# Kernel optimization log

Hardware: AMD Instinct MI355X
Metric: run time of the kernel (lower is better)

## Reference

```python
import jax, jax.numpy as jnp
import numpy as np

D_MODEL = 1024
D_FF = 4096
FFN_H = int(2 * D_FF / 3)  # 2730, per SwiGLUMLP
B, S = 4, 4096
LN_EPS = 1e-5
ATTN_EPS = 1e-6


def layer_norm(x, g, b):
    mu = jnp.mean(x, axis=-1, keepdims=True)
    var = jnp.mean(jnp.square(x - mu), axis=-1, keepdims=True)
    return (x - mu) * jax.lax.rsqrt(var + LN_EPS) * g + b


def setup_inputs() -> dict:
    key = jax.random.key(0)
    ks = jax.random.split(key, 16)
    s = 0.02
    return {
        "x": jax.random.normal(ks[0], (B, S, D_MODEL), dtype=jnp.float32),
        "Wqkv": jax.random.normal(ks[1], (D_MODEL, 3 * D_MODEL), dtype=jnp.float32) * s,
        "bqkv": jnp.zeros((3 * D_MODEL,), jnp.float32),
        "Wg": jax.random.normal(ks[2], (D_MODEL, FFN_H), dtype=jnp.float32) * s,
        "bg": jnp.zeros((FFN_H,), jnp.float32),
        "Wu": jax.random.normal(ks[3], (D_MODEL, FFN_H), dtype=jnp.float32) * s,
        "bu": jnp.zeros((FFN_H,), jnp.float32),
        "Wd": jax.random.normal(ks[4], (FFN_H, D_MODEL), dtype=jnp.float32) * s,
        "bd": jnp.zeros((D_MODEL,), jnp.float32),
        "g1": jnp.ones((D_MODEL,), jnp.float32),
        "b1": jnp.zeros((D_MODEL,), jnp.float32),
        "g2": jnp.ones((D_MODEL,), jnp.float32),
        "b2": jnp.zeros((D_MODEL,), jnp.float32),
    }


def reference(x, Wqkv, bqkv, Wg, bg, Wu, bu, Wd, bd, g1, b1, g2, b2):
    # QKV projection, split into q, k, v (each [B,S,D])
    qkv = jnp.einsum("bsd,de->bse", x, Wqkv) + bqkv
    q, k, v = jnp.split(qkv, 3, axis=-1)

    # Linear attention with elu(x)+1 feature map (non-causal)
    qp = jax.nn.elu(q) + 1.0
    kp = jax.nn.elu(k) + 1.0
    kv = jnp.einsum("bsd,bse->bde", kp, v)        # [B,D,D] context
    num = jnp.einsum("bsd,bde->bse", qp, kv)       # [B,S,D]
    k_sum = jnp.sum(kp, axis=1)                    # [B,D]
    den = jnp.einsum("bsd,bd->bs", qp, k_sum)[..., None]
    attn = num / (den + ATTN_EPS)

    x = layer_norm(x + attn, g1, b1)

    # SwiGLU MLP
    gate = jnp.einsum("bsd,dh->bsh", x, Wg) + bg
    up = jnp.einsum("bsd,dh->bsh", x, Wu) + bu
    ffn = jnp.einsum("bsh,hd->bsd", jax.nn.silu(gate) * up, Wd) + bd

    return layer_norm(x + ffn, g2, b2)
```

## Files before the change

kernel.cpp:

```cpp
#include <hip/hip_runtime.h>

#define SEQ 4096
#define TOK 16384
#define DM 1024
#define NQKV 3072
#define FFH 2730
#define FFHP 2816

typedef __bf16 bf16x8 __attribute__((ext_vector_type(8)));
typedef float f32x4 __attribute__((ext_vector_type(4)));

__device__ __forceinline__ unsigned short f2bf(float f) {
  union { float f; unsigned u; } v; v.f = f;
  unsigned r = v.u + 0x7fffu + ((v.u >> 16) & 1u);
  return (unsigned short)(r >> 16);
}
__device__ __forceinline__ float bf2f(unsigned short h) {
  union { unsigned u; float f; } v; v.u = ((unsigned)h) << 16;
  return v.f;
}

__device__ __forceinline__ void xcd_swizzle(int& bx, int& by) {
  const int gx = gridDim.x, gy = gridDim.y;
  const int chunk = gy >> 3;
  const int csh = __ffs(chunk) - 1;
  const int lin = by * gx + bx;
  const int xcd = lin & 7, j = lin >> 3;
  by = xcd * chunk + (j & (chunk - 1));
  bx = j >> csh;
}

enum { M_QKV = 0, M_BF16 = 1, M_NUM = 2, M_BIAS_F32 = 5 };

template<int MODE>
__global__ __launch_bounds__(256)
void gemm_kernel(const unsigned short* __restrict__ A,
                 const unsigned short* __restrict__ BT,
                 int K, int lda, int ldb, int ldc,
                 long zsA, long zsB, long zsC,
                 void* __restrict__ out0, void* __restrict__ out1, void* __restrict__ out2,
                 const float* __restrict__ bias, int nbias)
{
  __shared__ unsigned short As[2][128 * 64];
  __shared__ unsigned short Bs[2][128 * 64];
  const int tid  = threadIdx.x;
  const int wave = tid >> 6, lane = tid & 63;
  const int quad = lane >> 4, l16 = lane & 15;
  const int bz = blockIdx.z;
  int bx = blockIdx.x, by = blockIdx.y;
  xcd_swizzle(bx, by);

  const unsigned short* Ab = A + (size_t)zsA * bz + (size_t)by * 128 * lda;
  const unsigned short* Bb = BT + (size_t)zsB * bz + (size_t)bx * 128 * ldb;

  f32x4 acc[4][4] = {};

  const int srow   = lane >> 3;
  const int scol_g = (((lane & 7) ^ srow) * 8);
  const int axor   = l16 & 7;

  auto stage = [&](int buf, int k0) {
#pragma unroll
    for (int j = 0; j < 4; ++j) {
      int c = wave * 4 + j;
      const unsigned short* sa = Ab + (size_t)(c * 8 + srow) * lda + k0 + scol_g;
      __builtin_amdgcn_global_load_lds((__attribute__((address_space(1))) void*)sa,
          (__attribute__((address_space(3))) void*)(As[buf] + c * 512), 16, 0, 0);
      const unsigned short* sb = Bb + (size_t)(c * 8 + srow) * ldb + k0 + scol_g;
      __builtin_amdgcn_global_load_lds((__attribute__((address_space(1))) void*)sb,
          (__attribute__((address_space(3))) void*)(Bs[buf] + c * 512), 16, 0, 0);
    }
  };

  const int NIT = K >> 6;
  stage(0, 0);
  int cur = 0;
  for (int it = 0; it < NIT; ++it) {
    __builtin_amdgcn_s_waitcnt(0);
    __syncthreads();
    if (it + 1 < NIT) stage(cur ^ 1, (it + 1) << 6);
#pragma unroll
    for (int kk = 0; kk < 64; kk += 32) {
      bf16x8 af[4], bfr[4];
#pragma unroll
      for (int mt = 0; mt < 4; ++mt)
        af[mt] = *(const bf16x8*)(As[cur] + ((wave >> 1) * 64 + mt * 16 + l16) * 64
                                     + ((((kk >> 3) + quad) ^ axor) * 8));
#pragma unroll
      for (int nt = 0; nt < 4; ++nt)
        bfr[nt] = *(const bf16x8*)(Bs[cur] + ((wave & 1) * 64 + nt * 16 + l16) * 64
                                      + ((((kk >> 3) + quad) ^ axor) * 8));
#pragma unroll
      for (int mt = 0; mt < 4; ++mt)
#pragma unroll
        for (int nt = 0; nt < 4; ++nt)
          acc[mt][nt] = __builtin_amdgcn_mfma_f32_16x16x32_bf16(af[mt], bfr[nt], acc[mt][nt], 0, 0, 0);
    }
    cur ^= 1;
  }

#pragma unroll
  for (int mt = 0; mt < 4; ++mt) {
#pragma unroll
    for (int nt = 0; nt < 4; ++nt) {
      const int r0 = by * 128 + (wave >> 1) * 64 + mt * 16 + quad * 4;
      const int c  = bx * 128 + (wave & 1) * 64 + nt * 16 + l16;
      float vals[4];
#pragma unroll
      for (int i = 0; i < 4; ++i) vals[i] = acc[mt][nt][i];

      if (MODE == M_QKV) {
        const int b = r0 >> 12, s0 = r0 & 4095;
#pragma unroll
        for (int i = 0; i < 4; ++i) vals[i] += bias[c];
        if (c < 1024) {
#pragma unroll
          for (int i = 0; i < 4; ++i) {
            float e = vals[i] > 0.f ? vals[i] + 1.f : __expf(vals[i]);
            ((unsigned short*)out0)[(size_t)(r0 + i) * DM + c] = f2bf(e);
          }
        } else if (c < 2048) {
          ushort4 o;
          float e0 = vals[0] > 0.f ? vals[0] + 1.f : __expf(vals[0]);
          float e1 = vals[1] > 0.f ? vals[1] + 1.f : __expf(vals[1]);
          float e2 = vals[2] > 0.f ? vals[2] + 1.f : __expf(vals[2]);
          float e3 = vals[3] > 0.f ? vals[3] + 1.f : __expf(vals[3]);
          o.x = f2bf(e0); o.y = f2bf(e1); o.z = f2bf(e2); o.w = f2bf(e3);
          *(ushort4*)((unsigned short*)out1 + (size_t)b * DM * SEQ + (size_t)(c - 1024) * SEQ + s0) = o;
        } else {
          ushort4 o;
          o.x = f2bf(vals[0]); o.y = f2bf(vals[1]); o.z = f2bf(vals[2]); o.w = f2bf(vals[3]);
          *(ushort4*)((unsigned short*)out2 + (size_t)b * DM * SEQ + (size_t)(c - 2048) * SEQ + s0) = o;
        }
      } else {
#pragma unroll
        for (int i = 0; i < 4; ++i) {
          const int r = r0 + i;
          float val = vals[i];
          if (MODE == M_BF16 || MODE == M_NUM) {
            ((unsigned short*)out0)[(size_t)zsC * bz + (size_t)r * ldc + c] = f2bf(val);
          } else {
            if (c < nbias) val += bias[c];
            ((float*)out0)[(size_t)r * ldc + c] = val;
          }
        }
      }
    }
  }
}

enum { G_GATEUP = 0, G_NUM = 1, G_BIAS_F32 = 2, G_QKV = 3 };

#define MBAR() asm volatile("s_barrier" ::: "memory")
#define WAITV(N) asm volatile("s_waitcnt vmcnt(" #N ")" ::: "memory")

#define LDS_ALL(BUF) do {                                                     \
    _Pragma("unroll")                                                         \
    for (int mt = 0; mt < 4; ++mt) {                                          \
      _Pragma("unroll")                                                       \
      for (int k2 = 0; k2 < 2; ++k2)                                          \
        af[0][mt][k2] = *(const bf16x8*)(As[BUF] +                            \
            (wm * 128 + mt * 16 + l16) * 64 + (((k2 * 4 + quad) ^ axor) * 8));\
    }                                                                         \
    _Pragma("unroll")                                                         \
    for (int nt = 0; nt < 2; ++nt) {                                          \
      _Pragma("unroll")                                                       \
      for (int k2 = 0; k2 < 2; ++k2)                                          \
        bfr[0][nt][k2] = *(const bf16x8*)(Bs[BUF] +                           \
            (wn * 64 + nt * 16 + l16) * 64 + (((k2 * 4 + quad) ^ axor) * 8)); \
    }                                                                         \
    _Pragma("unroll")                                                         \
    for (int mt = 0; mt < 4; ++mt) {                                          \
      _Pragma("unroll")                                                       \
      for (int k2 = 0; k2 < 2; ++k2)                                          \
        af[1][mt][k2] = *(const bf16x8*)(As[BUF] +                            \
            (wm * 128 + (4 + mt) * 16 + l16) * 64 +                           \
            (((k2 * 4 + quad) ^ axor) * 8));                                  \
    }                                                                         \
    _Pragma("unroll")                                                         \
    for (int nt = 0; nt < 2; ++nt) {                                          \
      _Pragma("unroll")                                                       \
      for (int k2 = 0; k2 < 2; ++k2)                                          \
        bfr[1][nt][k2] = *(const bf16x8*)(Bs[BUF] +                           \
            (wn * 64 + (2 + nt) * 16 + l16) * 64 +                            \
            (((k2 * 4 + quad) ^ axor) * 8));                                  \
    }                                                                         \
  } while (0)

#define MMAQ(QM, QN) do {                                                     \
    _Pragma("unroll")                                                         \
    for (int mt = 0; mt < 4; ++mt) {                                          \
      _Pragma("unroll")                                                       \
      for (int nt = 0; nt < 2; ++nt) {                                        \
        _Pragma("unroll")                                                     \
        for (int k2 = 0; k2 < 2; ++k2)                                        \
          acc[(QM) * 4 + mt][(QN) * 2 + nt] =                                 \
              __builtin_amdgcn_mfma_f32_16x16x32_bf16(af[QM][mt][k2],         \
                  bfr[QN][nt][k2], acc[(QM) * 4 + mt][(QN) * 2 + nt], 0, 0, 0);\
      }                                                                       \
    }                                                                         \
  } while (0)

#define PHASE(QM, QN, STAGE) do {                                             \
    STAGE                                                                     \
    MBAR();                                                                   \
    __builtin_amdgcn_sched_barrier(0);                                        \
    __builtin_amdgcn_s_setprio(1);                                            \
    MMAQ(QM, QN);                                                             \
    __builtin_amdgcn_s_setprio(0);                                            \
    WAITV(6);                                                                 \
    MBAR();                                                                   \
  } while (0)

template<int MODE>
__global__ __launch_bounds__(512, 2)
void gemm256_kernel(const unsigned short* __restrict__ A,
                    const unsigned short* __restrict__ BT,
                    int K, int lda, int ldb, int ldc,
                    long zsA, long zsB, long zsC,
                    void* __restrict__ out0,
                    void* __restrict__ out1, void* __restrict__ out2,
                    const float* __restrict__ bias0,
                    const float* __restrict__ bias1,
                    int nbias)
{
  __shared__ unsigned short As[2][256 * 64];
  __shared__ unsigned short Bs[2][256 * 64];
  const int tid  = threadIdx.x;
  const int wave = tid >> 6, lane = tid & 63;
  const int quad = lane >> 4, l16 = lane & 15;
  const int wm = wave >> 2, wn = wave & 3;
  const int bz = blockIdx.z;
  int bx = blockIdx.x, by = blockIdx.y;
  xcd_swizzle(bx, by);

  const unsigned short* Ab = A + (size_t)zsA * bz + (size_t)by * 256 * lda;
  const unsigned short* Bb = BT + (size_t)zsB * bz + (size_t)bx * 256 * ldb;

  f32x4 acc[8][4] = {};

  const int srow = lane >> 3;
  const int sxor = ((lane & 7) ^ srow) * 8;
  const int axor = l16 & 7;

  const unsigned short* pA[2][2];
  const unsigned short* pB[2][2];
  int cA[2][2], cB[2][2];
#pragma unroll
  for (int part = 0; part < 2; ++part) {
#pragma unroll
    for (int j = 0; j < 2; ++j) {
      int idx = wave * 2 + j;
      int ca = ((idx & 8) ? idx + 8 : idx) + part * 8;
      int cb = (idx >> 2) * 8 + (idx & 3) + part * 4;
      cA[part][j] = ca; cB[part][j] = cb;
      pA[part][j] = Ab + (size_t)(ca * 8 + srow) * lda + sxor;
      pB[part][j] = Bb + (size_t)(cb * 8 + srow) * ldb + sxor;
    }
  }

  auto stageA = [&](int buf, int part, int tile) {
    const int k0 = tile << 6;
#pragma unroll
    for (int j = 0; j < 2; ++j)
      __builtin_amdgcn_global_load_lds(
          (__attribute__((address_space(1))) void*)(pA[part][j] + k0),
          (__attribute__((address_space(3))) void*)(As[buf] + cA[part][j] * 512), 16, 0, 0);
  };
  auto stageB = [&](int buf, int part, int tile) {
    const int k0 = tile << 6;
#pragma unroll
    for (int j = 0; j < 2; ++j)
      __builtin_amdgcn_global_load_lds(
          (__attribute__((address_space(1))) void*)(pB[part][j] + k0),
          (__attribute__((address_space(3))) void*)(Bs[buf] + cB[part][j] * 512), 16, 0, 0);
  };

  stageA(0, 0, 0); stageB(0, 0, 0); stageA(0, 1, 0); stageB(0, 1, 0);
  stageA(1, 0, 1); stageB(1, 0, 1); stageA(1, 1, 1);
  WAITV(6);
  MBAR();

  bf16x8 af[2][4][2], bfr[2][2][2];
  const int NT = K >> 6;
  for (int i = 0; i < NT; i += 2) {
    const int t2s = (i + 2 < NT), t3s = (i + 3 < NT);
    LDS_ALL(0);
    PHASE(0, 0, { stageB(1, 1, i + 1); });
    PHASE(1, 0, { if (t2s) stageA(0, 0, i + 2); });
    PHASE(1, 1, { if (t2s) stageB(0, 0, i + 2); });
    PHASE(0, 1, { if (t2s) stageA(0, 1, i + 2); });
    LDS_ALL(1);
    PHASE(0, 0, { if (t2s) stageB(0, 1, i + 2); });
    PHASE(1, 0, { if (t3s) stageA(1, 0, i + 3); });
    PHASE(1, 1, { if (t3s) stageB(1, 0, i + 3); });
    PHASE(0, 1, { if (t3s) stageA(1, 1, i + 3); });
  }

  if (MODE == G_GATEUP) {
#pragma unroll
    for (int mt = 0; mt < 8; ++mt) {
      const int r0 = by * 256 + wm * 128 + mt * 16 + quad * 4;
#pragma unroll
      for (int p = 0; p < 2; ++p) {
        const int hc = bx * 128 + wn * 32 + p * 16 + l16;
        const float bgv = (hc < nbias) ? bias0[hc] : 0.f;
        const float buv = (hc < nbias) ? bias1[hc] : 0.f;
#pragma unroll
        for (int i2 = 0; i2 < 4; ++i2) {
          float g = acc[mt][2 * p][i2] + bgv;
          float u = acc[mt][2 * p + 1][i2] + buv;
          float hv = g / (1.f + __expf(-g)) * u;
          ((unsigned short*)out0)[(size_t)(r0 + i2) * ldc + hc] = f2bf(hv);
        }
      }
    }
  } else {
#pragma unroll
    for (int mt = 0; mt < 8; ++mt) {
#pragma unroll
      for (int nt = 0; nt < 4; ++nt) {
        const int r0 = by * 256 + wm * 128 + mt * 16 + quad * 4;
        const int c  = bx * 256 + wn * 64 + nt * 16 + l16;
#pragma unroll
        for (int i2 = 0; i2 < 4; ++i2) {
          float v = acc[mt][nt][i2];
          if (MODE == G_NUM) {
            ((unsigned short*)out0)[(size_t)zsC * bz + (size_t)(r0 + i2) * ldc + c] = f2bf(v);
          } else {
            if (c < nbias) v += bias0[c];
            ((float*)out0)[(size_t)(r0 + i2) * ldc + c] = v;
          }
        }
      }
    }
  }
}

__global__ __launch_bounds__(256)
void cvt_kernel(const float* __restrict__ in, unsigned short* __restrict__ out, int n)
{
  int i = (blockIdx.x * 256 + threadIdx.x) * 4;
  if (i < n) {
    float4 v = *(const float4*)(in + i);
    ushort4 o;
    o.x = f2bf(v.x); o.y = f2bf(v.y); o.z = f2bf(v.z); o.w = f2bf(v.w);
    *(ushort4*)(out + i) = o;
  }
}

__global__ __launch_bounds__(256)
void wtrans_kernel(const float* __restrict__ in, unsigned short* __restrict__ out,
                   int R, int C, int Cpad, int Rpad, int omode)
{
  __shared__ float tile[32][33];
  int r0 = blockIdx.x * 32;
  int c0 = blockIdx.y * 32;
  int tid = threadIdx.x;
#pragma unroll
  for (int j = 0; j < 4; ++j) {
    int r = j * 8 + (tid >> 5), c = tid & 31;
    float v = 0.f;
    if (r0 + r < R && c0 + c < C) v = in[(size_t)(r0 + r) * C + c0 + c];
    tile[r][c] = v;
  }
  __syncthreads();
#pragma unroll
  for (int j = 0; j < 4; ++j) {
    int c = j * 8 + (tid >> 5), r = tid & 31;
    int oc = c0 + c;
    int orow = (omode == 0) ? oc
             : ((oc >> 4) * 32 + (oc & 15) + ((omode == 2) ? 16 : 0));
    out[(size_t)orow * Rpad + (r0 + r)] = f2bf(tile[r][c]);
  }
}

__device__ __forceinline__ float block_sum(float v, float* sm)
{
#pragma unroll
  for (int o = 32; o > 0; o >>= 1) v += __shfl_down(v, o, 64);
  int w = threadIdx.x >> 6;
  if ((threadIdx.x & 63) == 0) sm[w] = v;
  __syncthreads();
  float r = sm[0] + sm[1] + sm[2] + sm[3];
  __syncthreads();
  return r;
}

__global__ __launch_bounds__(256)
void ksum_kernel(const unsigned short* __restrict__ kpT, float* __restrict__ ksum)
{
  __shared__ float sm[4];
  int row = blockIdx.x;
  const ushort4* src = (const ushort4*)(kpT + (size_t)row * SEQ);
  float s = 0.f;
#pragma unroll
  for (int j = 0; j < 4; ++j) {
    ushort4 v = src[threadIdx.x + j * 256];
    s += bf2f(v.x) + bf2f(v.y) + bf2f(v.z) + bf2f(v.w);
  }
  float tot = block_sum(s, sm);
  if (threadIdx.x == 0) ksum[row] = tot;
}

__global__ __launch_bounds__(256)
void ln1_kernel(const unsigned short* __restrict__ xb16, const unsigned short* __restrict__ num16,
                const unsigned short* __restrict__ qp, const float* __restrict__ ksum,
                const float* __restrict__ g1, const float* __restrict__ b1,
                unsigned short* __restrict__ yb)
{
  __shared__ float sm[4];
  int t = blockIdx.x, tid = threadIdx.x, b = t >> 12;
  ushort4 xv = ((const ushort4*)(xb16 + (size_t)t * DM))[tid];
  ushort4 nv = ((const ushort4*)(num16 + (size_t)t * DM))[tid];
  ushort4 qv = ((const ushort4*)(qp + (size_t)t * DM))[tid];
  float4 kv = ((const float4*)(ksum + (size_t)b * DM))[tid];
  float q0 = bf2f(qv.x), q1 = bf2f(qv.y), q2 = bf2f(qv.z), q3 = bf2f(qv.w);
  float den = block_sum(q0 * kv.x + q1 * kv.y + q2 * kv.z + q3 * kv.w, sm);
  float inv = 1.f / (den + 1e-6f);
  float r0 = bf2f(xv.x) + bf2f(nv.x) * inv, r1 = bf2f(xv.y) + bf2f(nv.y) * inv;
  float r2 = bf2f(xv.z) + bf2f(nv.z) * inv, r3 = bf2f(xv.w) + bf2f(nv.w) * inv;
  float s1 = block_sum(r0 + r1 + r2 + r3, sm);
  float s2 = block_sum(r0 * r0 + r1 * r1 + r2 * r2 + r3 * r3, sm);
  float mu = s1 * (1.f / 1024.f);
  float var = s2 * (1.f / 1024.f) - mu * mu;
  float rs = rsqrtf(var + 1e-5f);
  float4 gv = ((const float4*)g1)[tid];
  float4 bv = ((const float4*)b1)[tid];
  ushort4 o;
  o.x = f2bf((r0 - mu) * rs * gv.x + bv.x);
  o.y = f2bf((r1 - mu) * rs * gv.y + bv.y);
  o.z = f2bf((r2 - mu) * rs * gv.z + bv.z);
  o.w = f2bf((r3 - mu) * rs * gv.w + bv.w);
  ((ushort4*)(yb + (size_t)t * DM))[tid] = o;
}

__global__ __launch_bounds__(256)
void ln2_kernel(const unsigned short* __restrict__ yb, const float* __restrict__ ffn,
                const float* __restrict__ g2, const float* __restrict__ b2,
                float* __restrict__ out)
{
  __shared__ float sm[4];
  int t = blockIdx.x, tid = threadIdx.x;
  ushort4 yv = ((const ushort4*)(yb + (size_t)t * DM))[tid];
  float4 fv = ((const float4*)(ffn + (size_t)t * DM))[tid];
  float r0 = bf2f(yv.x) + fv.x, r1 = bf2f(yv.y) + fv.y;
  float r2 = bf2f(yv.z) + fv.z, r3 = bf2f(yv.w) + fv.w;
  float s1 = block_sum(r0 + r1 + r2 + r3, sm);
  float s2 = block_sum(r0 * r0 + r1 * r1 + r2 * r2 + r3 * r3, sm);
  float mu = s1 * (1.f / 1024.f);
  float var = s2 * (1.f / 1024.f) - mu * mu;
  float rs = rsqrtf(var + 1e-5f);
  float4 gv = ((const float4*)g2)[tid];
  float4 bv = ((const float4*)b2)[tid];
  float4 o;
  o.x = (r0 - mu) * rs * gv.x + bv.x;
  o.y = (r1 - mu) * rs * gv.y + bv.y;
  o.z = (r2 - mu) * rs * gv.z + bv.z;
  o.w = (r3 - mu) * rs * gv.w + bv.w;
  ((float4*)(out + (size_t)t * DM))[tid] = o;
}

extern "C" void kernel_launch(void* const* d_in, const int* in_sizes, int n_in,
                              void* d_out, int out_size, void* d_ws, size_t ws_size,
                              hipStream_t stream)
{
  const float* x    = (const float*)d_in[0];
  const float* Wqkv = (const float*)d_in[1];
  const float* bqkv = (const float*)d_in[2];
  const float* Wg   = (const float*)d_in[3];
  const float* bg   = (const float*)d_in[4];
  const float* Wu   = (const float*)d_in[5];
  const float* bu   = (const float*)d_in[6];
  const float* Wd   = (const float*)d_in[7];
  const float* bd   = (const float*)d_in[8];
  const float* g1   = (const float*)d_in[9];
  const float* b1   = (const float*)d_in[10];
  const float* g2   = (const float*)d_in[11];
  const float* b2   = (const float*)d_in[12];
  float* out = (float*)d_out;

  char* ws = (char*)d_ws;
  size_t off = 0;
  auto alloc = [&](size_t bytes) {
    char* p = ws + off;
    off += (bytes + 255) & ~(size_t)255;
    return p;
  };
  unsigned short* WqkvT = (unsigned short*)alloc((size_t)NQKV * DM * 2);
  unsigned short* WguT  = (unsigned short*)alloc((size_t)2 * FFHP * DM * 2);
  unsigned short* WdT   = (unsigned short*)alloc((size_t)DM * FFHP * 2);
  float*          ksum  = (float*)alloc((size_t)4 * DM * 4);
  unsigned short* xbyb  = (unsigned short*)alloc((size_t)TOK * DM * 2);
  unsigned short* kvT   = (unsigned short*)alloc((size_t)4 * DM * DM * 2);
  char* R3 = alloc((size_t)3 * TOK * DM * 2);
  unsigned short* qp  = (unsigned short*)(R3);
  unsigned short* kpT = (unsigned short*)(R3 + (size_t)TOK * DM * 2);
  unsigned short* vT  = (unsigned short*)(R3 + (size_t)2 * TOK * DM * 2);
  unsigned short* hbuf = (unsigned short*)(R3);
  unsigned short* xb = xbyb;
  unsigned short* yb = xbyb;
  unsigned short* num = (unsigned short*)d_out;
  float* ffn = (float*)d_out;

  dim3 blk(256), blk5(512);

  cvt_kernel<<<dim3(TOK * DM / 1024), blk, 0, stream>>>(x, xb, TOK * DM);
  wtrans_kernel<<<dim3(32, 96), blk, 0, stream>>>(Wqkv, WqkvT, 1024, 3072, 3072, 1024, 0);
  wtrans_kernel<<<dim3(32, 88), blk, 0, stream>>>(Wg, WguT, 1024, FFH, FFHP, 1024, 1);
  wtrans_kernel<<<dim3(32, 88), blk, 0, stream>>>(Wu, WguT, 1024, FFH, FFHP, 1024, 2);
  wtrans_kernel<<<dim3(88, 32), blk, 0, stream>>>(Wd, WdT, FFH, 1024, 1024, FFHP, 0);
  gemm_kernel<M_QKV><<<dim3(NQKV / 128, TOK / 128), blk, 0, stream>>>(
      xb, WqkvT, 1024, 1024, 1024, 0, 0, 0, 0, qp, kpT, vT, bqkv, NQKV);
  ksum_kernel<<<dim3(4096), blk, 0, stream>>>(kpT, ksum);
  gemm_kernel<M_BF16><<<dim3(8, 8, 4), blk, 0, stream>>>(
      vT, kpT, 4096, 4096, 4096, 1024,
      (long)DM * SEQ, (long)DM * SEQ, (long)DM * DM,
      kvT, nullptr, nullptr, nullptr, 0);
  gemm256_kernel<G_NUM><<<dim3(4, 16, 4), blk5, 0, stream>>>(
      qp, kvT, 1024, 1024, 1024, 1024,
      (long)SEQ * DM, (long)DM * DM, (long)SEQ * DM,
      num, nullptr, nullptr, nullptr, nullptr, 0);
  ln1_kernel<<<dim3(TOK), blk, 0, stream>>>(xb, num, qp, ksum, g1, b1, yb);
  gemm256_kernel<G_GATEUP><<<dim3(2 * FFHP / 256, TOK / 256), blk5, 0, stream>>>(
      yb, WguT, 1024, DM, DM, FFHP, 0, 0, 0, hbuf, nullptr, nullptr, bg, bu, FFH);
  gemm256_kernel<G_BIAS_F32><<<dim3(DM / 256, TOK / 256), blk5, 0, stream>>>(
      hbuf, WdT, FFHP, FFHP, FFHP, DM, 0, 0, 0, ffn, nullptr, nullptr, bd, nullptr, DM);
  ln2_kernel<<<dim3(TOK), blk, 0, stream>>>(yb, ffn, g2, b2, out);

  (void)in_sizes; (void)n_in; (void)out_size; (void)ws_size;
}
```

Baseline: 821.0 us.

## Stage gate-up epilogue through LDS for coalesced stores; defer vmcnt waits

The SwiGLU epilogue of the gate/up GEMM now writes bf16 results into a swizzled LDS tile, then each thread stores 16-byte vectors of contiguous columns to global memory. This replaces scattered 2-byte stores. The pipeline also drops the vmcnt wait from every phase, keeping it only before the LDS reload at the end of each half-iteration, and drains fully on the last tiles. This aims to cut stall time inside the main loop, with a small risk of reading stale LDS if the staging order is wrong. Unused out1/out2 parameters and an enum value are removed.

```diff
diff --git a/kernel.cpp b/kernel.cpp
--- a/kernel.cpp
+++ b/kernel.cpp
@@ -9,6 +9,7 @@
 
 typedef __bf16 bf16x8 __attribute__((ext_vector_type(8)));
 typedef float f32x4 __attribute__((ext_vector_type(4)));
+typedef unsigned short u16x8 __attribute__((ext_vector_type(8)));
 
 __device__ __forceinline__ unsigned short f2bf(float f) {
   union { float f; unsigned u; } v; v.f = f;
@@ -149,7 +150,7 @@
   }
 }
 
-enum { G_GATEUP = 0, G_NUM = 1, G_BIAS_F32 = 2, G_QKV = 3 };
+enum { G_GATEUP = 0, G_NUM = 1, G_BIAS_F32 = 2 };
 
 #define MBAR() asm volatile("s_barrier" ::: "memory")
 #define WAITV(N) asm volatile("s_waitcnt vmcnt(" #N ")" ::: "memory")
@@ -201,14 +202,14 @@
     }                                                                         \
   } while (0)
 
-#define PHASE(QM, QN, STAGE) do {                                             \
+#define PHASE(QM, QN, STAGE, WAIT) do {                                       \
     STAGE                                                                     \
     MBAR();                                                                   \
     __builtin_amdgcn_sched_barrier(0);                                        \
     __builtin_amdgcn_s_setprio(1);                                            \
     MMAQ(QM, QN);                                                             \
     __builtin_amdgcn_s_setprio(0);                                            \
-    WAITV(6);                                                                 \
+    WAIT                                                                      \
     MBAR();                                                                   \
   } while (0)
 
@@ -219,7 +220,6 @@
                     int K, int lda, int ldb, int ldc,
                     long zsA, long zsB, long zsC,
                     void* __restrict__ out0,
-                    void* __restrict__ out1, void* __restrict__ out2,
                     const float* __restrict__ bias0,
                     const float* __restrict__ bias1,
                     int nbias)
@@ -286,24 +286,28 @@
   for (int i = 0; i < NT; i += 2) {
     const int t2s = (i + 2 < NT), t3s = (i + 3 < NT);
     LDS_ALL(0);
-    PHASE(0, 0, { stageB(1, 1, i + 1); });
-    PHASE(1, 0, { if (t2s) stageA(0, 0, i + 2); });
-    PHASE(1, 1, { if (t2s) stageB(0, 0, i + 2); });
-    PHASE(0, 1, { if (t2s) stageA(0, 1, i + 2); });
+    PHASE(0, 0, { stageB(1, 1, i + 1); }, {});
+    PHASE(1, 0, { if (t2s) stageA(0, 0, i + 2); }, {});
+    PHASE(1, 1, { if (t2s) stageB(0, 0, i + 2); }, {});
+    PHASE(0, 1, { if (t2s) stageA(0, 1, i + 2); },
+                { if (t2s) { WAITV(6); } else { WAITV(0); } });
     LDS_ALL(1);
-    PHASE(0, 0, { if (t2s) stageB(0, 1, i + 2); });
-    PHASE(1, 0, { if (t3s) stageA(1, 0, i + 3); });
-    PHASE(1, 1, { if (t3s) stageB(1, 0, i + 3); });
-    PHASE(0, 1, { if (t3s) stageA(1, 1, i + 3); });
+    PHASE(0, 0, { if (t2s) stageB(0, 1, i + 2); }, {});
+    PHASE(1, 0, { if (t3s) stageA(1, 0, i + 3); }, {});
+    PHASE(1, 1, { if (t3s) stageB(1, 0, i + 3); }, {});
+    PHASE(0, 1, { if (t3s) stageA(1, 1, i + 3); },
+                { if (t2s) { WAITV(6); } else { WAITV(0); } });
   }
 
   if (MODE == G_GATEUP) {
+    unsigned short* lf16 = (unsigned short*)As;
 #pragma unroll
     for (int mt = 0; mt < 8; ++mt) {
-      const int r0 = by * 256 + wm * 128 + mt * 16 + quad * 4;
+      const int rloc = wm * 128 + mt * 16 + quad * 4;
 #pragma unroll
       for (int p = 0; p < 2; ++p) {
-        const int hc = bx * 128 + wn * 32 + p * 16 + l16;
+        const int cloc = wn * 32 + p * 16 + l16;
+        const int hc = bx * 128 + cloc;
         const float bgv = (hc < nbias) ? bias0[hc] : 0.f;
         const float buv = (hc < nbias) ? bias1[hc] : 0.f;
 #pragma unroll
@@ -311,8 +315,21 @@
           float g = acc[mt][2 * p][i2] + bgv;
           float u = acc[mt][2 * p + 1][i2] + buv;
           float hv = g / (1.f + __expf(-g)) * u;
-          ((unsigned short*)out0)[(size_t)(r0 + i2) * ldc + hc] = f2bf(hv);
+          const int r = rloc + i2;
+          lf16[r * 128 + (cloc ^ (((r >> 2) & 3) << 4))] = f2bf(hv);
         }
+      }
+    }
+    __syncthreads();
+    {
+      const int cb = (tid & 15) * 8;
+      const int rb = (tid >> 4) * 8;
+#pragma unroll
+      for (int j = 0; j < 8; ++j) {
+        const int r = rb + j;
+        const int cs = cb ^ (((r >> 2) & 3) << 4);
+        u16x8 v = *(const u16x8*)(lf16 + r * 128 + cs);
+        *(u16x8*)((unsigned short*)out0 + (size_t)(by * 256 + r) * ldc + bx * 128 + cb) = v;
       }
     }
   } else {
@@ -520,12 +537,12 @@
   gemm256_kernel<G_NUM><<<dim3(4, 16, 4), blk5, 0, stream>>>(
       qp, kvT, 1024, 1024, 1024, 1024,
       (long)SEQ * DM, (long)DM * DM, (long)SEQ * DM,
-      num, nullptr, nullptr, nullptr, nullptr, 0);
+      num, nullptr, nullptr, 0);
   ln1_kernel<<<dim3(TOK), blk, 0, stream>>>(xb, num, qp, ksum, g1, b1, yb);
   gemm256_kernel<G_GATEUP><<<dim3(2 * FFHP / 256, TOK / 256), blk5, 0, stream>>>(
-      yb, WguT, 1024, DM, DM, FFHP, 0, 0, 0, hbuf, nullptr, nullptr, bg, bu, FFH);
+      yb, WguT, 1024, DM, DM, FFHP, 0, 0, 0, hbuf, bg, bu, FFH);
   gemm256_kernel<G_BIAS_F32><<<dim3(DM / 256, TOK / 256), blk5, 0, stream>>>(
-      hbuf, WdT, FFHP, FFHP, FFHP, DM, 0, 0, 0, ffn, nullptr, nullptr, bd, nullptr, DM);
+      hbuf, WdT, FFHP, FFHP, FFHP, DM, 0, 0, 0, ffn, bd, nullptr, DM);
   ln2_kernel<<<dim3(TOK), blk, 0, stream>>>(yb, ffn, g2, b2, out);
 
   (void)in_sizes; (void)n_in; (void)out_size; (void)ws_size;
```

New measurement: 839.1 us. 1.02x slower.
